# Kernel optimization log

Hardware: AMD Instinct MI355X
Metric: run time of the kernel (lower is better)

The kernel has to match this reference:

```python
import jax, jax.numpy as jnp
import numpy as np

N, E = 32, 512          # graphs per batch, padded nodes per graph
IN_DIM = 128            # in_dim
OUT_DIM = 64            # out_dim (d)
N_TYPE = 3              # config.num_edge_type
Q_DIM = 128             # config.input_dim (q_update=False)


def setup_inputs() -> dict:
    key = jax.random.key(0)
    ks = jax.random.split(key, 8)
    s = 0.05  # weight init scale (stands in for xavier_uniform)
    return {
        "input_state": jax.random.normal(ks[0], (N, E, IN_DIM), jnp.float32),
        "adj": jax.random.randint(ks[1], (N, E, E), 0, N_TYPE + 1, jnp.int32),
        "query_vec": jax.random.normal(ks[2], (N, Q_DIM), jnp.float32),
        "node_mask": jax.random.uniform(ks[3], (N, E, 1), jnp.float32),
        "W_type": jax.random.normal(ks[4], (N_TYPE, IN_DIM, OUT_DIM), jnp.float32) * s,
        "a_type": jax.random.normal(ks[5], (N_TYPE, 2 * OUT_DIM, 1), jnp.float32) * s,
        "qattn_W1": jax.random.normal(ks[6], (N_TYPE, Q_DIM, 2 * OUT_DIM), jnp.float32) * s,
        "qattn_W2": jax.random.normal(ks[7], (N_TYPE, 2 * OUT_DIM, 2 * OUT_DIM), jnp.float32) * s,
    }


def reference(input_state, adj, query_vec, node_mask, W_type, a_type, qattn_W1, qattn_W2):
    # Per-type node projections: (T, N, E, d). Dropout omitted (eval mode, p=0).
    h_all = jnp.einsum("nei,tio->tneo", input_state, W_type)

    # Query gate per type: sigmoid(relu(q @ W1) @ W2) -> (T, N, 2d)
    qg = jax.nn.relu(jnp.einsum("nq,tqc->tnc", query_vec, qattn_W1))
    qg = jax.nn.sigmoid(jnp.einsum("tnc,tcd->tnd", qg, qattn_W2))

    d = h_all.shape[-1]
    a_src = a_type[:, :d, 0]   # (T, d) applied to the repeated (source) half
    a_dst = a_type[:, d:, 0]   # (T, d) applied to the tiled (target) half

    # score[t,n,i,j] = lrelu( (h[t,n,i]*qg1[t,n]) . a_src[t] + (h[t,n,j]*qg2[t,n]) . a_dst[t] )
    # This is exactly cat([h_i, h_j]) * q_gate @ a without materializing (N,E,E,2d).
    s_src = jnp.einsum("tned,tnd,td->tne", h_all, qg[..., :d], a_src)
    s_dst = jnp.einsum("tned,tnd,td->tne", h_all, qg[..., d:], a_dst)
    score = jax.nn.leaky_relu(s_src[:, :, :, None] + s_dst[:, :, None, :], 0.2)  # (T,N,E,E)

    # Accumulate scores where adj matches each edge type (1-indexed).
    type_ids = jnp.arange(1, N_TYPE + 1, dtype=adj.dtype)[:, None, None, None]
    scores = jnp.sum(jnp.where(adj[None] == type_ids, score, 0.0), axis=0)  # (N,E,E)

    # Mask non-edges and softmax over dim=2 (target nodes).
    scores = jnp.where(adj > 0, scores, jnp.float32(-1e30))
    coefs = jax.nn.softmax(scores, axis=2)

    # h from the last edge-type loop iteration, node-masked.
    h = h_all[-1] * node_mask  # (N,E,d)

    # out[n,j,:] = sum_i coefs[n,i,j] * h[n,i,:]  (sum over dim=1 in the torch code)
    return jnp.einsum("nij,nid->njd", coefs, h)
```

## Files before the change

kernel.cpp:

```cpp
#include <hip/hip_runtime.h>
#include <hip/hip_bf16.h>

#define N_G 32
#define E_N 512
#define IN_D 128
#define OUT_D 64
#define NT 3
#define Q_D 128

#define WS_WSRC 0
#define WS_WDST 12288
#define WS_SSRC 24576
#define WS_SDST 73728
#define WS_RINV 139264
#define WS_H    155648
#define WS_W2T  679936
#define WS_ADJ2 684032

typedef const float* fp;
typedef __attribute__((ext_vector_type(8))) short short8x;
typedef __attribute__((ext_vector_type(4))) float float4x;

static __device__ inline ushort f2bf(float x) {
  __hip_bfloat16 b = __float2bfloat16(x);
  return *(ushort*)&b;
}
static __device__ inline float bf2f(ushort u) {
  return __uint_as_float((uint)u << 16);
}

__global__ __launch_bounds__(512) void k1_qgate(fp qv_g, fp Wt, fp at,
                                                fp W1, fp W2,
                                                float* __restrict__ ws) {
  const int tb = blockIdx.x >> 5;
  const int n  = blockIdx.x & 31;
  __shared__ float qv[128];
  __shared__ float ps[16][132];
  __shared__ float g1s[128], g2s[128];
  __shared__ float gsv[64], gdv[64];
  const int t  = threadIdx.x;
  const int h  = t >> 5;
  const int cg = (t & 31) << 2;

  if (t < 128) qv[t] = qv_g[n * Q_D + t];
  __syncthreads();

  {
    float a0 = 0.f, a1 = 0.f, a2 = 0.f, a3 = 0.f;
    const float* Wp = W1 + tb * 16384 + (h * 8) * 128 + cg;
    #pragma unroll
    for (int q = 0; q < 8; q++) {
      float4 wv = *(const float4*)(Wp + q * 128);
      float qq = qv[h * 8 + q];
      a0 += qq * wv.x; a1 += qq * wv.y; a2 += qq * wv.z; a3 += qq * wv.w;
    }
    ps[h][cg + 0] = a0; ps[h][cg + 1] = a1;
    ps[h][cg + 2] = a2; ps[h][cg + 3] = a3;
  }
  __syncthreads();
  if (t < 128) {
    float s = 0.f;
    #pragma unroll
    for (int k = 0; k < 16; k++) s += ps[k][t];
    g1s[t] = s > 0.f ? s : 0.f;
  }
  __syncthreads();

  {
    float a0 = 0.f, a1 = 0.f, a2 = 0.f, a3 = 0.f;
    const float* Wp = W2 + tb * 16384 + (h * 8) * 128 + cg;
    #pragma unroll
    for (int q = 0; q < 8; q++) {
      float4 wv = *(const float4*)(Wp + q * 128);
      float qq = g1s[h * 8 + q];
      a0 += qq * wv.x; a1 += qq * wv.y; a2 += qq * wv.z; a3 += qq * wv.w;
    }
    ps[h][cg + 0] = a0; ps[h][cg + 1] = a1;
    ps[h][cg + 2] = a2; ps[h][cg + 3] = a3;
  }
  __syncthreads();
  if (t < 128) {
    float s = 0.f;
    #pragma unroll
    for (int k = 0; k < 16; k++) s += ps[k][t];
    g2s[t] = 1.f / (1.f + __expf(-s));
  }
  __syncthreads();
  if (t < 64) {
    gsv[t] = g2s[t] * at[tb * 128 + t];
    gdv[t] = g2s[64 + t] * at[tb * 128 + 64 + t];
  }
  __syncthreads();

  if (t < 256) {
    const int i = t & 127, hf = t >> 7;
    float as = 0.f, ad = 0.f;
    const float* Wp = Wt + tb * 8192 + i * 64 + hf * 32;
    #pragma unroll
    for (int dj = 0; dj < 8; dj++) {
      float4 wv = *(const float4*)(Wp + dj * 4);
      const float* gp = gsv + hf * 32 + dj * 4;
      const float* gq = gdv + hf * 32 + dj * 4;
      as += wv.x * gp[0] + wv.y * gp[1] + wv.z * gp[2] + wv.w * gp[3];
      ad += wv.x * gq[0] + wv.y * gq[1] + wv.z * gq[2] + wv.w * gq[3];
    }
    ps[hf][i]     = as;
    ps[2 + hf][i] = ad;
  }
  __syncthreads();
  if (t < 128) {
    ws[WS_WSRC + tb * 4096 + n * 128 + t] = ps[0][t] + ps[1][t];
    ws[WS_WDST + tb * 4096 + n * 128 + t] = ps[2][t] + ps[3][t];
  }

  if (tb == 2 && t < 128) {
    int f = n * 256 + t * 2;
    int d = f >> 7, i0 = f & 127;
    uint lo = f2bf(Wt[2 * 8192 + i0 * 64 + d]);
    uint hi = f2bf(Wt[2 * 8192 + (i0 + 1) * 64 + d]);
    ((uint*)(ws + WS_W2T))[f >> 1] = lo | (hi << 16);
  }
}

__global__ __launch_bounds__(256) void k2_h_s(fp X, fp mask,
                                              float* __restrict__ ws) {
  const int n  = blockIdx.x >> 4;
  const int e0 = (blockIdx.x & 15) << 5;
  __shared__ ushort A[32 * 136];
  __shared__ ushort BT[64 * 136];
  __shared__ ushort eT[64 * 40];
  __shared__ float wv[6 * 128];
  const int t = threadIdx.x;
  ushort* hb = (ushort*)(ws + WS_H);
  const ushort* w2t = (const ushort*)(ws + WS_W2T);

  #pragma unroll
  for (int k = 0; k < 4; k++) {
    int f = t + 256 * k;
    int e = f >> 5, iq = f & 31;
    float4 v = *(const float4*)&X[(n * E_N + e0 + e) * IN_D + iq * 4];
    uint2 pk;
    pk.x = (uint)f2bf(v.x) | ((uint)f2bf(v.y) << 16);
    pk.y = (uint)f2bf(v.z) | ((uint)f2bf(v.w) << 16);
    *(uint2*)&A[e * 136 + iq * 4] = pk;
  }
  #pragma unroll
  for (int k = 0; k < 4; k++) {
    int f = t + 256 * k;
    int d = f >> 4, iq8 = f & 15;
    *(uint4*)&BT[d * 136 + iq8 * 8] = *(const uint4*)&w2t[d * 128 + iq8 * 8];
  }
  #pragma unroll
  for (int k = 0; k < 3; k++) {
    int idx = t + 256 * k;
    int row = idx >> 7, i = idx & 127;
    wv[idx] = (row < 3) ? ws[WS_WSRC + row * 4096 + n * 128 + i]
                        : ws[WS_WDST + (row - 3) * 4096 + n * 128 + i];
  }
  __syncthreads();

  const int w = t >> 6, lane = t & 63;
  const int m15 = lane & 15, quad = lane >> 4;
  const int msub = w & 1, dhalf = w >> 1;

  float4x acc2[2];
  acc2[0] = (float4x)(0.f); acc2[1] = (float4x)(0.f);
  #pragma unroll
  for (int ks = 0; ks < 4; ks++) {
    short8x af = *(const short8x*)&A[(msub * 16 + m15) * 136 + ks * 32 + quad * 8];
    #pragma unroll
    for (int dd = 0; dd < 2; dd++) {
      short8x bfv = *(const short8x*)&BT[((dhalf * 2 + dd) * 16 + m15) * 136 + ks * 32 + quad * 8];
      acc2[dd] = __builtin_amdgcn_mfma_f32_16x16x32_bf16(af, bfv, acc2[dd], 0, 0, 0);
    }
  }

  if (t < 192) {
    const int e = t / 6, q = t % 6;
    float acc = 0.f;
    #pragma unroll
    for (int i8 = 0; i8 < 16; i8++) {
      uint4 pk = *(const uint4*)&A[e * 136 + i8 * 8];
      const float* wp = &wv[q * 128 + i8 * 8];
      acc += bf2f((ushort)(pk.x & 0xffff)) * wp[0];
      acc += bf2f((ushort)(pk.x >> 16))    * wp[1];
      acc += bf2f((ushort)(pk.y & 0xffff)) * wp[2];
      acc += bf2f((ushort)(pk.y >> 16))    * wp[3];
      acc += bf2f((ushort)(pk.z & 0xffff)) * wp[4];
      acc += bf2f((ushort)(pk.z >> 16))    * wp[5];
      acc += bf2f((ushort)(pk.w & 0xffff)) * wp[6];
      acc += bf2f((ushort)(pk.w >> 16))    * wp[7];
    }
    if (q < 3) ws[WS_SSRC + q * 16384 + n * 512 + e0 + e] = acc;
    else       ws[WS_SDST + (q - 3) * 16384 + n * 512 + e0 + e] = acc;
  }

  float mv[4];
  #pragma unroll
  for (int rg = 0; rg < 4; rg++)
    mv[rg] = mask[n * E_N + e0 + msub * 16 + quad * 4 + rg];
  #pragma unroll
  for (int dd = 0; dd < 2; dd++) {
    int dRow = (dhalf * 2 + dd) * 16 + m15;
    #pragma unroll
    for (int rg = 0; rg < 4; rg++) {
      int e = msub * 16 + quad * 4 + rg;
      eT[dRow * 40 + e] = f2bf(acc2[dd][rg] * mv[rg]);
    }
  }
  __syncthreads();

  {
    int d = t >> 2, e8 = t & 3;
    *(uint4*)&hb[(n * 64 + d) * 512 + e0 + e8 * 8] =
        *(const uint4*)&eT[d * 40 + e8 * 8];
  }
}

__global__ __launch_bounds__(256) void k3_rowstats(const int* __restrict__ adj,
                                                   float* __restrict__ ws) {
  const int n  = blockIdx.x >> 7;
  const int ib = blockIdx.x & 127;
  __shared__ float sd[3 * 512];
  const int t = threadIdx.x;
  ushort* adj2 = (ushort*)(ws + WS_ADJ2);

  #pragma unroll
  for (int k = 0; k < 6; k++) {
    int idx = t + 256 * k;
    sd[idx] = ws[WS_SDST + (idx >> 9) * 16384 + n * 512 + (idx & 511)];
  }
  __syncthreads();

  const int wave = t >> 6, lane = t & 63;
  const int i = ib * 4 + wave;
  const float s0 = ws[WS_SSRC + 0 * 16384 + n * 512 + i];
  const float s1 = ws[WS_SSRC + 1 * 16384 + n * 512 + i];
  const float s2 = ws[WS_SSRC + 2 * 16384 + n * 512 + i];
  const int* arow = &adj[(n * E_N + i) * E_N];

  float sum = 0.f;
  uint pack = 0;
  #pragma unroll
  for (int b = 0; b < 8; b++) {
    int j = b * 64 + lane;
    int a = arow[j];
    pack |= (uint)(a & 3) << (2 * b);
    if (a > 0) {
      float s = (a == 1) ? s0 : (a == 2 ? s1 : s2);
      float v = s + sd[(a - 1) * 512 + j];
      v = v > 0.f ? v : 0.2f * v;
      sum += __expf(v);
    }
  }
  #pragma unroll
  for (int off = 32; off >= 1; off >>= 1) sum += __shfl_xor(sum, off, 64);
  if (lane == 0) ws[WS_RINV + n * 512 + i] = 1.f / sum;
  adj2[(n * E_N + i) * 64 + lane] = (ushort)pack;
}

__global__ __launch_bounds__(256) void k4_out(float* __restrict__ ws,
                                              float* __restrict__ out) {
  const int n  = blockIdx.x >> 4;
  const int j0 = (blockIdx.x & 15) << 5;
  __shared__ ushort cT[32 * 136];
  __shared__ ushort hT[64 * 136];
  __shared__ ushort aS[128 * 64];
  __shared__ float sdT[3 * 32];
  __shared__ float ssT[3 * 128];
  __shared__ float riT[128];
  const int t = threadIdx.x;
  const ushort* hb = (const ushort*)(ws + WS_H);
  const ushort* adj2 = (const ushort*)(ws + WS_ADJ2);

  if (t < 96) sdT[t] = ws[WS_SDST + (t >> 5) * 16384 + n * 512 + j0 + (t & 31)];

  const int w = t >> 6, lane = t & 63;
  const int m15 = lane & 15, quad = lane >> 4;
  const int msub = w & 1, dhalf = w >> 1;
  const int c   = t & 31;
  const int rpb = t >> 5;
  const int u     = (j0 & 63) + c;
  const int shift = 2 * (j0 >> 6);

  float4x acc[2];
  acc[0] = (float4x)(0.f); acc[1] = (float4x)(0.f);

  for (int it = 0; it < 4; it++) {
    const int i0 = it << 7;

    #pragma unroll
    for (int k = 0; k < 4; k++) {
      int f = t + 256 * k;
      int d = f >> 4, i16 = f & 15;
      *(uint4*)&hT[d * 136 + i16 * 8] =
          *(const uint4*)&hb[(n * 64 + d) * 512 + i0 + i16 * 8];
    }
    #pragma unroll
    for (int k = 0; k < 4; k++) {
      int f = t + 256 * k;
      int r = f >> 3, c8 = f & 7;
      *(uint4*)&aS[r * 64 + c8 * 8] =
          *(const uint4*)&adj2[(size_t)(n * E_N + i0 + r) * 64 + c8 * 8];
    }
    #pragma unroll
    for (int k = 0; k < 2; k++) {
      int idx = t + 256 * k;
      if (idx < 128) riT[idx] = ws[WS_RINV + n * 512 + i0 + idx];
      else {
        int j2 = idx - 128;
        ssT[j2] = ws[WS_SSRC + (j2 >> 7) * 16384 + n * 512 + i0 + (j2 & 127)];
      }
    }
    __syncthreads();

    #pragma unroll
    for (int k = 0; k < 8; k++) {
      int r0 = 2 * (rpb + 8 * k);
      uint pack = 0;
      int a = (aS[r0 * 64 + u] >> shift) & 3;
      if (a > 0) {
        float v = ssT[(a - 1) * 128 + r0] + sdT[(a - 1) * 32 + c];
        v = v > 0.f ? v : 0.2f * v;
        pack = f2bf(__expf(v) * riT[r0]);
      }
      a = (aS[(r0 + 1) * 64 + u] >> shift) & 3;
      if (a > 0) {
        float v = ssT[(a - 1) * 128 + r0 + 1] + sdT[(a - 1) * 32 + c];
        v = v > 0.f ? v : 0.2f * v;
        pack |= (uint)f2bf(__expf(v) * riT[r0 + 1]) << 16;
      }
      *(uint*)&cT[c * 136 + r0] = pack;
    }
    __syncthreads();

    #pragma unroll
    for (int ks = 0; ks < 4; ks++) {
      short8x af = *(const short8x*)&cT[(msub * 16 + m15) * 136 + ks * 32 + quad * 8];
      #pragma unroll
      for (int dd = 0; dd < 2; dd++) {
        short8x bfv = *(const short8x*)&hT[((dhalf * 2 + dd) * 16 + m15) * 136 + ks * 32 + quad * 8];
        acc[dd] = __builtin_amdgcn_mfma_f32_16x16x32_bf16(af, bfv, acc[dd], 0, 0, 0);
      }
    }
    __syncthreads();
  }

  #pragma unroll
  for (int dd = 0; dd < 2; dd++)
    #pragma unroll
    for (int rg = 0; rg < 4; rg++) {
      int j = j0 + msub * 16 + quad * 4 + rg;
      out[(n * E_N + j) * 64 + (dhalf * 2 + dd) * 16 + m15] = acc[dd][rg];
    }
}

extern "C" void kernel_launch(void* const* d_in, const int* in_sizes, int n_in,
                              void* d_out, int out_size, void* d_ws, size_t ws_size,
                              hipStream_t stream) {
  fp input_state  = (fp)d_in[0];
  const int* adj  = (const int*)d_in[1];
  fp query_vec    = (fp)d_in[2];
  fp node_mask    = (fp)d_in[3];
  fp W_type       = (fp)d_in[4];
  fp a_type       = (fp)d_in[5];
  fp qattn_W1     = (fp)d_in[6];
  fp qattn_W2     = (fp)d_in[7];
  float* out = (float*)d_out;
  float* ws  = (float*)d_ws;

  k1_qgate<<<96, 512, 0, stream>>>(query_vec, W_type, a_type, qattn_W1, qattn_W2, ws);
  k2_h_s<<<512, 256, 0, stream>>>(input_state, node_mask, ws);
  k3_rowstats<<<32 * 128, 256, 0, stream>>>(adj, ws);
  k4_out<<<32 * 16, 256, 0, stream>>>(ws, out);
}
```

Baseline: 123.6 us.

## Fuse four stage kernels into one cooperative kernel with grid-wide barriers

New measurement: 448.2 us. 263% more time.

```diff
diff --git a/kernel.cpp b/kernel.cpp
--- a/kernel.cpp
+++ b/kernel.cpp
@@ -1,5 +1,8 @@
 #include <hip/hip_runtime.h>
 #include <hip/hip_bf16.h>
+#include <hip/hip_cooperative_groups.h>
+
+namespace cgx = cooperative_groups;
 
 #define N_G 32
 #define E_N 512
@@ -29,348 +32,362 @@
   return __uint_as_float((uint)u << 16);
 }
 
-__global__ __launch_bounds__(512) void k1_qgate(fp qv_g, fp Wt, fp at,
-                                                fp W1, fp W2,
-                                                float* __restrict__ ws) {
-  const int tb = blockIdx.x >> 5;
-  const int n  = blockIdx.x & 31;
-  __shared__ float qv[128];
-  __shared__ float ps[16][132];
-  __shared__ float g1s[128], g2s[128];
-  __shared__ float gsv[64], gdv[64];
-  const int t  = threadIdx.x;
-  const int h  = t >> 5;
-  const int cg = (t & 31) << 2;
-
-  if (t < 128) qv[t] = qv_g[n * Q_D + t];
-  __syncthreads();
+__global__ __launch_bounds__(256, 2) void fused_gat(
+    fp X, const int* __restrict__ adj, fp qv_g, fp mask,
+    fp Wt, fp at, fp W1, fp W2,
+    float* __restrict__ out, float* __restrict__ ws) {
+  cgx::grid_group grid = cgx::this_grid();
+  __shared__ alignas(16) char smem[45056];
+  const int b = blockIdx.x;
+  const int t = threadIdx.x;
+
+  if (b < 96) {
+    const int tb = b >> 5;
+    const int n  = b & 31;
+    float* qv  = (float*)smem;
+    float* ps  = (float*)(smem + 512);
+    float* g1s = (float*)(smem + 4736);
+    float* g2s = (float*)(smem + 5248);
+    float* gsv = (float*)(smem + 5760);
+    float* gdv = (float*)(smem + 6016);
+    const int h   = t >> 5;
+    const int cg_ = (t & 31) << 2;
+
+    if (t < 128) qv[t] = qv_g[n * Q_D + t];
+    __syncthreads();
+
+    {
+      float a0 = 0.f, a1 = 0.f, a2 = 0.f, a3 = 0.f;
+      const float* Wp = W1 + tb * 16384 + (h * 16) * 128 + cg_;
+      #pragma unroll
+      for (int q = 0; q < 16; q++) {
+        float4 wv4 = *(const float4*)(Wp + q * 128);
+        float qq = qv[h * 16 + q];
+        a0 += qq * wv4.x; a1 += qq * wv4.y; a2 += qq * wv4.z; a3 += qq * wv4.w;
+      }
+      ps[h * 132 + cg_ + 0] = a0; ps[h * 132 + cg_ + 1] = a1;
+      ps[h * 132 + cg_ + 2] = a2; ps[h * 132 + cg_ + 3] = a3;
+    }
+    __syncthreads();
+    if (t < 128) {
+      float s = 0.f;
+      #pragma unroll
+      for (int k = 0; k < 8; k++) s += ps[k * 132 + t];
+      g1s[t] = s > 0.f ? s : 0.f;
+    }
+    __syncthreads();
+
+    {
+      float a0 = 0.f, a1 = 0.f, a2 = 0.f, a3 = 0.f;
+      const float* Wp = W2 + tb * 16384 + (h * 16) * 128 + cg_;
+      #pragma unroll
+      for (int q = 0; q < 16; q++) {
+        float4 wv4 = *(const float4*)(Wp + q * 128);
+        float qq = g1s[h * 16 + q];
+        a0 += qq * wv4.x; a1 += qq * wv4.y; a2 += qq * wv4.z; a3 += qq * wv4.w;
+      }
+      ps[h * 132 + cg_ + 0] = a0; ps[h * 132 + cg_ + 1] = a1;
+      ps[h * 132 + cg_ + 2] = a2; ps[h * 132 + cg_ + 3] = a3;
+    }
+    __syncthreads();
+    if (t < 128) {
+      float s = 0.f;
+      #pragma unroll
+      for (int k = 0; k < 8; k++) s += ps[k * 132 + t];
+      g2s[t] = 1.f / (1.f + __expf(-s));
+    }
+    __syncthreads();
+    if (t < 64) {
+      gsv[t] = g2s[t] * at[tb * 128 + t];
+      gdv[t] = g2s[64 + t] * at[tb * 128 + 64 + t];
+    }
+    __syncthreads();
+
+    {
+      const int i = t & 127, hf = t >> 7;
+      float as = 0.f, ad = 0.f;
+      const float* Wp = Wt + tb * 8192 + i * 64 + hf * 32;
+      #pragma unroll
+      for (int dj = 0; dj < 8; dj++) {
+        float4 wv4 = *(const float4*)(Wp + dj * 4);
+        const float* gp = gsv + hf * 32 + dj * 4;
+        const float* gq = gdv + hf * 32 + dj * 4;
+        as += wv4.x * gp[0] + wv4.y * gp[1] + wv4.z * gp[2] + wv4.w * gp[3];
+        ad += wv4.x * gq[0] + wv4.y * gq[1] + wv4.z * gq[2] + wv4.w * gq[3];
+      }
+      ps[hf * 132 + i]       = as;
+      ps[(2 + hf) * 132 + i] = ad;
+    }
+    __syncthreads();
+    if (t < 128) {
+      ws[WS_WSRC + tb * 4096 + n * 128 + t] = ps[0 * 132 + t] + ps[1 * 132 + t];
+      ws[WS_WDST + tb * 4096 + n * 128 + t] = ps[2 * 132 + t] + ps[3 * 132 + t];
+    }
+    if (tb == 2 && t < 128) {
+      int f = n * 256 + t * 2;
+      int d = f >> 7, i0 = f & 127;
+      uint lo = f2bf(Wt[2 * 8192 + i0 * 64 + d]);
+      uint hi = f2bf(Wt[2 * 8192 + (i0 + 1) * 64 + d]);
+      ((uint*)(ws + WS_W2T))[f >> 1] = lo | (hi << 16);
+    }
+  }
+
+  __threadfence();
+  grid.sync();
 
   {
-    float a0 = 0.f, a1 = 0.f, a2 = 0.f, a3 = 0.f;
-    const float* Wp = W1 + tb * 16384 + (h * 8) * 128 + cg;
-    #pragma unroll
-    for (int q = 0; q < 8; q++) {
-      float4 wv = *(const float4*)(Wp + q * 128);
-      float qq = qv[h * 8 + q];
-      a0 += qq * wv.x; a1 += qq * wv.y; a2 += qq * wv.z; a3 += qq * wv.w;
-    }
-    ps[h][cg + 0] = a0; ps[h][cg + 1] = a1;
-    ps[h][cg + 2] = a2; ps[h][cg + 3] = a3;
-  }
-  __syncthreads();
-  if (t < 128) {
-    float s = 0.f;
-    #pragma unroll
-    for (int k = 0; k < 16; k++) s += ps[k][t];
-    g1s[t] = s > 0.f ? s : 0.f;
-  }
-  __syncthreads();
-
-  {
-    float a0 = 0.f, a1 = 0.f, a2 = 0.f, a3 = 0.f;
-    const float* Wp = W2 + tb * 16384 + (h * 8) * 128 + cg;
-    #pragma unroll
-    for (int q = 0; q < 8; q++) {
-      float4 wv = *(const float4*)(Wp + q * 128);
-      float qq = g1s[h * 8 + q];
-      a0 += qq * wv.x; a1 += qq * wv.y; a2 += qq * wv.z; a3 += qq * wv.w;
-    }
-    ps[h][cg + 0] = a0; ps[h][cg + 1] = a1;
-    ps[h][cg + 2] = a2; ps[h][cg + 3] = a3;
-  }
-  __syncthreads();
-  if (t < 128) {
-    float s = 0.f;
-    #pragma unroll
-    for (int k = 0; k < 16; k++) s += ps[k][t];
-    g2s[t] = 1.f / (1.f + __expf(-s));
-  }
-  __syncthreads();
-  if (t < 64) {
-    gsv[t] = g2s[t] * at[tb * 128 + t];
-    gdv[t] = g2s[64 + t] * at[tb * 128 + 64 + t];
-  }
-  __syncthreads();
-
-  if (t < 256) {
-    const int i = t & 127, hf = t >> 7;
-    float as = 0.f, ad = 0.f;
-    const float* Wp = Wt + tb * 8192 + i * 64 + hf * 32;
-    #pragma unroll
-    for (int dj = 0; dj < 8; dj++) {
-      float4 wv = *(const float4*)(Wp + dj * 4);
-      const float* gp = gsv + hf * 32 + dj * 4;
-      const float* gq = gdv + hf * 32 + dj * 4;
-      as += wv.x * gp[0] + wv.y * gp[1] + wv.z * gp[2] + wv.w * gp[3];
-      ad += wv.x * gq[0] + wv.y * gq[1] + wv.z * gq[2] + wv.w * gq[3];
-    }
-    ps[hf][i]     = as;
-    ps[2 + hf][i] = ad;
-  }
-  __syncthreads();
-  if (t < 128) {
-    ws[WS_WSRC + tb * 4096 + n * 128 + t] = ps[0][t] + ps[1][t];
-    ws[WS_WDST + tb * 4096 + n * 128 + t] = ps[2][t] + ps[3][t];
-  }
-
-  if (tb == 2 && t < 128) {
-    int f = n * 256 + t * 2;
-    int d = f >> 7, i0 = f & 127;
-    uint lo = f2bf(Wt[2 * 8192 + i0 * 64 + d]);
-    uint hi = f2bf(Wt[2 * 8192 + (i0 + 1) * 64 + d]);
-    ((uint*)(ws + WS_W2T))[f >> 1] = lo | (hi << 16);
-  }
-}
-
-__global__ __launch_bounds__(256) void k2_h_s(fp X, fp mask,
-                                              float* __restrict__ ws) {
-  const int n  = blockIdx.x >> 4;
-  const int e0 = (blockIdx.x & 15) << 5;
-  __shared__ ushort A[32 * 136];
-  __shared__ ushort BT[64 * 136];
-  __shared__ ushort eT[64 * 40];
-  __shared__ float wv[6 * 128];
-  const int t = threadIdx.x;
-  ushort* hb = (ushort*)(ws + WS_H);
-  const ushort* w2t = (const ushort*)(ws + WS_W2T);
-
-  #pragma unroll
-  for (int k = 0; k < 4; k++) {
-    int f = t + 256 * k;
-    int e = f >> 5, iq = f & 31;
-    float4 v = *(const float4*)&X[(n * E_N + e0 + e) * IN_D + iq * 4];
-    uint2 pk;
-    pk.x = (uint)f2bf(v.x) | ((uint)f2bf(v.y) << 16);
-    pk.y = (uint)f2bf(v.z) | ((uint)f2bf(v.w) << 16);
-    *(uint2*)&A[e * 136 + iq * 4] = pk;
-  }
-  #pragma unroll
-  for (int k = 0; k < 4; k++) {
-    int f = t + 256 * k;
-    int d = f >> 4, iq8 = f & 15;
-    *(uint4*)&BT[d * 136 + iq8 * 8] = *(const uint4*)&w2t[d * 128 + iq8 * 8];
-  }
-  #pragma unroll
-  for (int k = 0; k < 3; k++) {
-    int idx = t + 256 * k;
-    int row = idx >> 7, i = idx & 127;
-    wv[idx] = (row < 3) ? ws[WS_WSRC + row * 4096 + n * 128 + i]
-                        : ws[WS_WDST + (row - 3) * 4096 + n * 128 + i];
-  }
-  __syncthreads();
-
-  const int w = t >> 6, lane = t & 63;
-  const int m15 = lane & 15, quad = lane >> 4;
-  const int msub = w & 1, dhalf = w >> 1;
-
-  float4x acc2[2];
-  acc2[0] = (float4x)(0.f); acc2[1] = (float4x)(0.f);
-  #pragma unroll
-  for (int ks = 0; ks < 4; ks++) {
-    short8x af = *(const short8x*)&A[(msub * 16 + m15) * 136 + ks * 32 + quad * 8];
-    #pragma unroll
-    for (int dd = 0; dd < 2; dd++) {
-      short8x bfv = *(const short8x*)&BT[((dhalf * 2 + dd) * 16 + m15) * 136 + ks * 32 + quad * 8];
-      acc2[dd] = __builtin_amdgcn_mfma_f32_16x16x32_bf16(af, bfv, acc2[dd], 0, 0, 0);
-    }
-  }
-
-  if (t < 192) {
-    const int e = t / 6, q = t % 6;
-    float acc = 0.f;
-    #pragma unroll
-    for (int i8 = 0; i8 < 16; i8++) {
-      uint4 pk = *(const uint4*)&A[e * 136 + i8 * 8];
-      const float* wp = &wv[q * 128 + i8 * 8];
-      acc += bf2f((ushort)(pk.x & 0xffff)) * wp[0];
-      acc += bf2f((ushort)(pk.x >> 16))    * wp[1];
-      acc += bf2f((ushort)(pk.y & 0xffff)) * wp[2];
-      acc += bf2f((ushort)(pk.y >> 16))    * wp[3];
-      acc += bf2f((ushort)(pk.z & 0xffff)) * wp[4];
-      acc += bf2f((ushort)(pk.z >> 16))    * wp[5];
-      acc += bf2f((ushort)(pk.w & 0xffff)) * wp[6];
-      acc += bf2f((ushort)(pk.w >> 16))    * wp[7];
-    }
-    if (q < 3) ws[WS_SSRC + q * 16384 + n * 512 + e0 + e] = acc;
-    else       ws[WS_SDST + (q - 3) * 16384 + n * 512 + e0 + e] = acc;
-  }
-
-  float mv[4];
-  #pragma unroll
-  for (int rg = 0; rg < 4; rg++)
-    mv[rg] = mask[n * E_N + e0 + msub * 16 + quad * 4 + rg];
-  #pragma unroll
-  for (int dd = 0; dd < 2; dd++) {
-    int dRow = (dhalf * 2 + dd) * 16 + m15;
-    #pragma unroll
-    for (int rg = 0; rg < 4; rg++) {
-      int e = msub * 16 + quad * 4 + rg;
-      eT[dRow * 40 + e] = f2bf(acc2[dd][rg] * mv[rg]);
-    }
-  }
-  __syncthreads();
-
-  {
-    int d = t >> 2, e8 = t & 3;
-    *(uint4*)&hb[(n * 64 + d) * 512 + e0 + e8 * 8] =
-        *(const uint4*)&eT[d * 40 + e8 * 8];
-  }
-}
-
-__global__ __launch_bounds__(256) void k3_rowstats(const int* __restrict__ adj,
-                                                   float* __restrict__ ws) {
-  const int n  = blockIdx.x >> 7;
-  const int ib = blockIdx.x & 127;
-  __shared__ float sd[3 * 512];
-  const int t = threadIdx.x;
-  ushort* adj2 = (ushort*)(ws + WS_ADJ2);
-
-  #pragma unroll
-  for (int k = 0; k < 6; k++) {
-    int idx = t + 256 * k;
-    sd[idx] = ws[WS_SDST + (idx >> 9) * 16384 + n * 512 + (idx & 511)];
-  }
-  __syncthreads();
-
-  const int wave = t >> 6, lane = t & 63;
-  const int i = ib * 4 + wave;
-  const float s0 = ws[WS_SSRC + 0 * 16384 + n * 512 + i];
-  const float s1 = ws[WS_SSRC + 1 * 16384 + n * 512 + i];
-  const float s2 = ws[WS_SSRC + 2 * 16384 + n * 512 + i];
-  const int* arow = &adj[(n * E_N + i) * E_N];
-
-  float sum = 0.f;
-  uint pack = 0;
-  #pragma unroll
-  for (int b = 0; b < 8; b++) {
-    int j = b * 64 + lane;
-    int a = arow[j];
-    pack |= (uint)(a & 3) << (2 * b);
-    if (a > 0) {
-      float s = (a == 1) ? s0 : (a == 2 ? s1 : s2);
-      float v = s + sd[(a - 1) * 512 + j];
-      v = v > 0.f ? v : 0.2f * v;
-      sum += __expf(v);
-    }
-  }
-  #pragma unroll
-  for (int off = 32; off >= 1; off >>= 1) sum += __shfl_xor(sum, off, 64);
-  if (lane == 0) ws[WS_RINV + n * 512 + i] = 1.f / sum;
-  adj2[(n * E_N + i) * 64 + lane] = (ushort)pack;
-}
-
-__global__ __launch_bounds__(256) void k4_out(float* __restrict__ ws,
-                                              float* __restrict__ out) {
-  const int n  = blockIdx.x >> 4;
-  const int j0 = (blockIdx.x & 15) << 5;
-  __shared__ ushort cT[32 * 136];
-  __shared__ ushort hT[64 * 136];
-  __shared__ ushort aS[128 * 64];
-  __shared__ float sdT[3 * 32];
-  __shared__ float ssT[3 * 128];
-  __shared__ float riT[128];
-  const int t = threadIdx.x;
-  const ushort* hb = (const ushort*)(ws + WS_H);
-  const ushort* adj2 = (const ushort*)(ws + WS_ADJ2);
-
-  if (t < 96) sdT[t] = ws[WS_SDST + (t >> 5) * 16384 + n * 512 + j0 + (t & 31)];
-
-  const int w = t >> 6, lane = t & 63;
-  const int m15 = lane & 15, quad = lane >> 4;
-  const int msub = w & 1, dhalf = w >> 1;
-  const int c   = t & 31;
-  const int rpb = t >> 5;
-  const int u     = (j0 & 63) + c;
-  const int shift = 2 * (j0 >> 6);
-
-  float4x acc[2];
-  acc[0] = (float4x)(0.f); acc[1] = (float4x)(0.f);
-
-  for (int it = 0; it < 4; it++) {
-    const int i0 = it << 7;
+    const int n  = b >> 4;
+    const int e0 = (b & 15) << 5;
+    ushort* A   = (ushort*)smem;
+    ushort* BT  = (ushort*)(smem + 8704);
+    ushort* eTl = (ushort*)(smem + 26112);
+    float*  wv  = (float*)(smem + 31232);
+    ushort* hb = (ushort*)(ws + WS_H);
+    const ushort* w2t = (const ushort*)(ws + WS_W2T);
 
     #pragma unroll
     for (int k = 0; k < 4; k++) {
       int f = t + 256 * k;
-      int d = f >> 4, i16 = f & 15;
-      *(uint4*)&hT[d * 136 + i16 * 8] =
-          *(const uint4*)&hb[(n * 64 + d) * 512 + i0 + i16 * 8];
+      int e = f >> 5, iq = f & 31;
+      float4 v = *(const float4*)&X[(n * E_N + e0 + e) * IN_D + iq * 4];
+      uint2 pk;
+      pk.x = (uint)f2bf(v.x) | ((uint)f2bf(v.y) << 16);
+      pk.y = (uint)f2bf(v.z) | ((uint)f2bf(v.w) << 16);
+      *(uint2*)&A[e * 136 + iq * 4] = pk;
     }
     #pragma unroll
     for (int k = 0; k < 4; k++) {
       int f = t + 256 * k;
-      int r = f >> 3, c8 = f & 7;
-      *(uint4*)&aS[r * 64 + c8 * 8] =
-          *(const uint4*)&adj2[(size_t)(n * E_N + i0 + r) * 64 + c8 * 8];
-    }
-    #pragma unroll
-    for (int k = 0; k < 2; k++) {
+      int d = f >> 4, iq8 = f & 15;
+      *(uint4*)&BT[d * 136 + iq8 * 8] = *(const uint4*)&w2t[d * 128 + iq8 * 8];
+    }
+    #pragma unroll
+    for (int k = 0; k < 3; k++) {
       int idx = t + 256 * k;
-      if (idx < 128) riT[idx] = ws[WS_RINV + n * 512 + i0 + idx];
-      else {
-        int j2 = idx - 128;
-        ssT[j2] = ws[WS_SSRC + (j2 >> 7) * 16384 + n * 512 + i0 + (j2 & 127)];
-      }
-    }
-    __syncthreads();
-
-    #pragma unroll
-    for (int k = 0; k < 8; k++) {
-      int r0 = 2 * (rpb + 8 * k);
+      int row = idx >> 7, i = idx & 127;
+      wv[idx] = (row < 3) ? ws[WS_WSRC + row * 4096 + n * 128 + i]
+                          : ws[WS_WDST + (row - 3) * 4096 + n * 128 + i];
+    }
+    __syncthreads();
+
+    const int w = t >> 6, lane = t & 63;
+    const int m15 = lane & 15, quad = lane >> 4;
+    const int msub = w & 1, dhalf = w >> 1;
+
+    float4x acc2[2];
+    acc2[0] = (float4x)(0.f); acc2[1] = (float4x)(0.f);
+    #pragma unroll
+    for (int ks = 0; ks < 4; ks++) {
+      short8x af = *(const short8x*)&A[(msub * 16 + m15) * 136 + ks * 32 + quad * 8];
+      #pragma unroll
+      for (int dd = 0; dd < 2; dd++) {
+        short8x bfv = *(const short8x*)&BT[((dhalf * 2 + dd) * 16 + m15) * 136 + ks * 32 + quad * 8];
+        acc2[dd] = __builtin_amdgcn_mfma_f32_16x16x32_bf16(af, bfv, acc2[dd], 0, 0, 0);
+      }
+    }
+
+    if (t < 192) {
+      const int e = t / 6, q = t % 6;
+      float acc = 0.f;
+      #pragma unroll
+      for (int i8 = 0; i8 < 16; i8++) {
+        uint4 pk = *(const uint4*)&A[e * 136 + i8 * 8];
+        const float* wp = &wv[q * 128 + i8 * 8];
+        acc += bf2f((ushort)(pk.x & 0xffff)) * wp[0];
+        acc += bf2f((ushort)(pk.x >> 16))    * wp[1];
+        acc += bf2f((ushort)(pk.y & 0xffff)) * wp[2];
+        acc += bf2f((ushort)(pk.y >> 16))    * wp[3];
+        acc += bf2f((ushort)(pk.z & 0xffff)) * wp[4];
+        acc += bf2f((ushort)(pk.z >> 16))    * wp[5];
+        acc += bf2f((ushort)(pk.w & 0xffff)) * wp[6];
+        acc += bf2f((ushort)(pk.w >> 16))    * wp[7];
+      }
+      if (q < 3) ws[WS_SSRC + q * 16384 + n * 512 + e0 + e] = acc;
+      else       ws[WS_SDST + (q - 3) * 16384 + n * 512 + e0 + e] = acc;
+    }
+
+    float mv[4];
+    #pragma unroll
+    for (int rg = 0; rg < 4; rg++)
+      mv[rg] = mask[n * E_N + e0 + msub * 16 + quad * 4 + rg];
+    #pragma unroll
+    for (int dd = 0; dd < 2; dd++) {
+      int dRow = (dhalf * 2 + dd) * 16 + m15;
+      #pragma unroll
+      for (int rg = 0; rg < 4; rg++) {
+        int e = msub * 16 + quad * 4 + rg;
+        eTl[dRow * 40 + e] = f2bf(acc2[dd][rg] * mv[rg]);
+      }
+    }
+    __syncthreads();
+
+    {
+      int d = t >> 2, e8 = t & 3;
+      *(uint4*)&hb[(n * 64 + d) * 512 + e0 + e8 * 8] =
+          *(const uint4*)&eTl[d * 40 + e8 * 8];
+    }
+  }
+
+  __threadfence();
+  grid.sync();
+
+  {
+    const int n  = b >> 4;
+    const int rb = (b & 15) << 5;
+    float* sd = (float*)smem;
+    ushort* adj2 = (ushort*)(ws + WS_ADJ2);
+
+    #pragma unroll
+    for (int k = 0; k < 6; k++) {
+      int idx = t + 256 * k;
+      sd[idx] = ws[WS_SDST + (idx >> 9) * 16384 + n * 512 + (idx & 511)];
+    }
+    __syncthreads();
+
+    const int wave = t >> 6, lane = t & 63;
+    for (int rr = 0; rr < 8; rr++) {
+      const int i = rb + wave * 8 + rr;
+      const float s0 = ws[WS_SSRC + 0 * 16384 + n * 512 + i];
+      const float s1 = ws[WS_SSRC + 1 * 16384 + n * 512 + i];
+      const float s2 = ws[WS_SSRC + 2 * 16384 + n * 512 + i];
+      const int* arow = &adj[(n * E_N + i) * E_N];
+
+      float sum = 0.f;
       uint pack = 0;
-      int a = (aS[r0 * 64 + u] >> shift) & 3;
-      if (a > 0) {
-        float v = ssT[(a - 1) * 128 + r0] + sdT[(a - 1) * 32 + c];
-        v = v > 0.f ? v : 0.2f * v;
-        pack = f2bf(__expf(v) * riT[r0]);
-      }
-      a = (aS[(r0 + 1) * 64 + u] >> shift) & 3;
-      if (a > 0) {
-        float v = ssT[(a - 1) * 128 + r0 + 1] + sdT[(a - 1) * 32 + c];
-        v = v > 0.f ? v : 0.2f * v;
-        pack |= (uint)f2bf(__expf(v) * riT[r0 + 1]) << 16;
-      }
-      *(uint*)&cT[c * 136 + r0] = pack;
-    }
-    __syncthreads();
-
-    #pragma unroll
-    for (int ks = 0; ks < 4; ks++) {
-      short8x af = *(const short8x*)&cT[(msub * 16 + m15) * 136 + ks * 32 + quad * 8];
-      #pragma unroll
-      for (int dd = 0; dd < 2; dd++) {
-        short8x bfv = *(const short8x*)&hT[((dhalf * 2 + dd) * 16 + m15) * 136 + ks * 32 + quad * 8];
-        acc[dd] = __builtin_amdgcn_mfma_f32_16x16x32_bf16(af, bfv, acc[dd], 0, 0, 0);
-      }
-    }
-    __syncthreads();
+      #pragma unroll
+      for (int bb = 0; bb < 8; bb++) {
+        int j = bb * 64 + lane;
+        int a = arow[j];
+        pack |= (uint)(a & 3) << (2 * bb);
+        if (a > 0) {
+          float s = (a == 1) ? s0 : (a == 2 ? s1 : s2);
+          float v = s + sd[(a - 1) * 512 + j];
+          v = v > 0.f ? v : 0.2f * v;
+          sum += __expf(v);
+        }
+      }
+      #pragma unroll
+      for (int off = 32; off >= 1; off >>= 1) sum += __shfl_xor(sum, off, 64);
+      if (lane == 0) ws[WS_RINV + n * 512 + i] = 1.f / sum;
+      adj2[(n * E_N + i) * 64 + lane] = (ushort)pack;
+    }
   }
 
-  #pragma unroll
-  for (int dd = 0; dd < 2; dd++)
-    #pragma unroll
-    for (int rg = 0; rg < 4; rg++) {
-      int j = j0 + msub * 16 + quad * 4 + rg;
-      out[(n * E_N + j) * 64 + (dhalf * 2 + dd) * 16 + m15] = acc[dd][rg];
-    }
+  __threadfence();
+  grid.sync();
+
+  {
+    const int n  = b >> 4;
+    const int j0 = (b & 15) << 5;
+    ushort* cT = (ushort*)smem;
+    ushort* hT = (ushort*)(smem + 8704);
+    ushort* aS = (ushort*)(smem + 26112);
+    float* sdT = (float*)(smem + 42496);
+    float* ssT = (float*)(smem + 42880);
+    float* riT = (float*)(smem + 44416);
+    const ushort* hb = (const ushort*)(ws + WS_H);
+    const ushort* adj2 = (const ushort*)(ws + WS_ADJ2);
+
+    if (t < 96) sdT[t] = ws[WS_SDST + (t >> 5) * 16384 + n * 512 + j0 + (t & 31)];
+
+    const int w = t >> 6, lane = t & 63;
+    const int m15 = lane & 15, quad = lane >> 4;
+    const int msub = w & 1, dhalf = w >> 1;
+    const int c   = t & 31;
+    const int rpb = t >> 5;
+    const int u     = (j0 & 63) + c;
+    const int shift = 2 * (j0 >> 6);
+
+    float4x acc[2];
+    acc[0] = (float4x)(0.f); acc[1] = (float4x)(0.f);
+
+    for (int it = 0; it < 4; it++) {
+      const int i0 = it << 7;
+
+      #pragma unroll
+      for (int k = 0; k < 4; k++) {
+        int f = t + 256 * k;
+        int d = f >> 4, i16 = f & 15;
+        *(uint4*)&hT[d * 136 + i16 * 8] =
+            *(const uint4*)&hb[(n * 64 + d) * 512 + i0 + i16 * 8];
+      }
+      #pragma unroll
+      for (int k = 0; k < 4; k++) {
+        int f = t + 256 * k;
+        int r = f >> 3, c8 = f & 7;
+        *(uint4*)&aS[r * 64 + c8 * 8] =
+            *(const uint4*)&adj2[(size_t)(n * E_N + i0 + r) * 64 + c8 * 8];
+      }
+      #pragma unroll
+      for (int k = 0; k < 2; k++) {
+        int idx = t + 256 * k;
+        if (idx < 128) riT[idx] = ws[WS_RINV + n * 512 + i0 + idx];
+        else {
+          int j2 = idx - 128;
+          ssT[j2] = ws[WS_SSRC + (j2 >> 7) * 16384 + n * 512 + i0 + (j2 & 127)];
+        }
+      }
+      __syncthreads();
+
+      #pragma unroll
+      for (int k = 0; k < 8; k++) {
+        int r0 = 2 * (rpb + 8 * k);
+        uint pack = 0;
+        int a = (aS[r0 * 64 + u] >> shift) & 3;
+        if (a > 0) {
+          float v = ssT[(a - 1) * 128 + r0] + sdT[(a - 1) * 32 + c];
+          v = v > 0.f ? v : 0.2f * v;
+          pack = f2bf(__expf(v) * riT[r0]);
+        }
+        a = (aS[(r0 + 1) * 64 + u] >> shift) & 3;
+        if (a > 0) {
+          float v = ssT[(a - 1) * 128 + r0 + 1] + sdT[(a - 1) * 32 + c];
+          v = v > 0.f ? v : 0.2f * v;
+          pack |= (uint)f2bf(__expf(v) * riT[r0 + 1]) << 16;
+        }
+        *(uint*)&cT[c * 136 + r0] = pack;
+      }
+      __syncthreads();
+
+      #pragma unroll
+      for (int ks = 0; ks < 4; ks++) {
+        short8x af = *(const short8x*)&cT[(msub * 16 + m15) * 136 + ks * 32 + quad * 8];
+        #pragma unroll
+        for (int dd = 0; dd < 2; dd++) {
+          short8x bfv = *(const short8x*)&hT[((dhalf * 2 + dd) * 16 + m15) * 136 + ks * 32 + quad * 8];
+          acc[dd] = __builtin_amdgcn_mfma_f32_16x16x32_bf16(af, bfv, acc[dd], 0, 0, 0);
+        }
+      }
+      __syncthreads();
+    }
+
+    #pragma unroll
+    for (int dd = 0; dd < 2; dd++)
+      #pragma unroll
+      for (int rg = 0; rg < 4; rg++) {
+        int j = j0 + msub * 16 + quad * 4 + rg;
+        out[(n * E_N + j) * 64 + (dhalf * 2 + dd) * 16 + m15] = acc[dd][rg];
+      }
+  }
 }
 
 extern "C" void kernel_launch(void* const* d_in, const int* in_sizes, int n_in,
                               void* d_out, int out_size, void* d_ws, size_t ws_size,
                               hipStream_t stream) {
-  fp input_state  = (fp)d_in[0];
-  const int* adj  = (const int*)d_in[1];
-  fp query_vec    = (fp)d_in[2];
-  fp node_mask    = (fp)d_in[3];
-  fp W_type       = (fp)d_in[4];
-  fp a_type       = (fp)d_in[5];
-  fp qattn_W1     = (fp)d_in[6];
-  fp qattn_W2     = (fp)d_in[7];
+  const float* input_state = (const float*)d_in[0];
+  const int*   adj         = (const int*)d_in[1];
+  const float* query_vec   = (const float*)d_in[2];
+  const float* node_mask   = (const float*)d_in[3];
+  const float* W_type      = (const float*)d_in[4];
+  const float* a_type      = (const float*)d_in[5];
+  const float* qattn_W1    = (const float*)d_in[6];
+  const float* qattn_W2    = (const float*)d_in[7];
   float* out = (float*)d_out;
   float* ws  = (float*)d_ws;
 
-  k1_qgate<<<96, 512, 0, stream>>>(query_vec, W_type, a_type, qattn_W1, qattn_W2, ws);
-  k2_h_s<<<512, 256, 0, stream>>>(input_state, node_mask, ws);
-  k3_rowstats<<<32 * 128, 256, 0, stream>>>(adj, ws);
-  k4_out<<<32 * 16, 256, 0, stream>>>(ws, out);
+  void* args[] = {(void*)&input_state, (void*)&adj, (void*)&query_vec,
+                  (void*)&node_mask, (void*)&W_type, (void*)&a_type,
+                  (void*)&qattn_W1, (void*)&qattn_W2, (void*)&out, (void*)&ws};
+  hipLaunchCooperativeKernel((const void*)fused_gat, dim3(512), dim3(256),
+                             args, 0, stream);
 }
```

## Move adjacency packing into qgate kernel and batch row stats per block

Applied to the files above, without the earlier changes.

Result: slower. 128.2 us (+3.7%).

```diff
diff --git a/kernel.cpp b/kernel.cpp
--- a/kernel.cpp
+++ b/kernel.cpp
@@ -29,60 +29,76 @@
   return __uint_as_float((uint)u << 16);
 }
 
-__global__ __launch_bounds__(512) void k1_qgate(fp qv_g, fp Wt, fp at,
-                                                fp W1, fp W2,
-                                                float* __restrict__ ws) {
-  const int tb = blockIdx.x >> 5;
-  const int n  = blockIdx.x & 31;
+__global__ __launch_bounds__(256) void k1_qgate_pack(
+    fp qv_g, fp Wt, fp at, fp W1, fp W2,
+    const int* __restrict__ adj, float* __restrict__ ws) {
+  const int b = blockIdx.x;
+  const int t = threadIdx.x;
+
+  if (b >= 96) {
+    const int w = t >> 6, lane = t & 63;
+    const int R = (b - 96) * 4 + w;
+    const int* arow = adj + (size_t)R * E_N;
+    uint pack = 0;
+    #pragma unroll
+    for (int bb = 0; bb < 8; bb++) {
+      int a = arow[bb * 64 + lane];
+      pack |= (uint)(a & 3) << (2 * bb);
+    }
+    ((ushort*)(ws + WS_ADJ2))[(size_t)R * 64 + lane] = (ushort)pack;
+    return;
+  }
+
+  const int tb = b >> 5;
+  const int n  = b & 31;
   __shared__ float qv[128];
-  __shared__ float ps[16][132];
+  __shared__ float ps[8][132];
   __shared__ float g1s[128], g2s[128];
   __shared__ float gsv[64], gdv[64];
-  const int t  = threadIdx.x;
-  const int h  = t >> 5;
-  const int cg = (t & 31) << 2;
+  const int h   = t >> 5;
+  const int cg_ = (t & 31) << 2;
 
   if (t < 128) qv[t] = qv_g[n * Q_D + t];
   __syncthreads();
 
   {
     float a0 = 0.f, a1 = 0.f, a2 = 0.f, a3 = 0.f;
-    const float* Wp = W1 + tb * 16384 + (h * 8) * 128 + cg;
-    #pragma unroll
-    for (int q = 0; q < 8; q++) {
-      float4 wv = *(const float4*)(Wp + q * 128);
-      float qq = qv[h * 8 + q];
-      a0 += qq * wv.x; a1 += qq * wv.y; a2 += qq * wv.z; a3 += qq * wv.w;
-    }
-    ps[h][cg + 0] = a0; ps[h][cg + 1] = a1;
-    ps[h][cg + 2] = a2; ps[h][cg + 3] = a3;
+    const float* Wp = W1 + tb * 16384 + (h * 16) * 128 + cg_;
+    #pragma unroll
+    for (int q = 0; q < 16; q++) {
+      float4 wv4 = *(const float4*)(Wp + q * 128);
+      float qq = qv[h * 16 + q];
+      a0 += qq * wv4.x; a1 += qq * wv4.y; a2 += qq * wv4.z; a3 += qq * wv4.w;
+    }
+    ps[h][cg_ + 0] = a0; ps[h][cg_ + 1] = a1;
+    ps[h][cg_ + 2] = a2; ps[h][cg_ + 3] = a3;
   }
   __syncthreads();
   if (t < 128) {
     float s = 0.f;
     #pragma unroll
-    for (int k = 0; k < 16; k++) s += ps[k][t];
+    for (int k = 0; k < 8; k++) s += ps[k][t];
     g1s[t] = s > 0.f ? s : 0.f;
   }
   __syncthreads();
 
   {
     float a0 = 0.f, a1 = 0.f, a2 = 0.f, a3 = 0.f;
-    const float* Wp = W2 + tb * 16384 + (h * 8) * 128 + cg;
-    #pragma unroll
-    for (int q = 0; q < 8; q++) {
-      float4 wv = *(const float4*)(Wp + q * 128);
-      float qq = g1s[h * 8 + q];
-      a0 += qq * wv.x; a1 += qq * wv.y; a2 += qq * wv.z; a3 += qq * wv.w;
-    }
-    ps[h][cg + 0] = a0; ps[h][cg + 1] = a1;
-    ps[h][cg + 2] = a2; ps[h][cg + 3] = a3;
+    const float* Wp = W2 + tb * 16384 + (h * 16) * 128 + cg_;
+    #pragma unroll
+    for (int q = 0; q < 16; q++) {
+      float4 wv4 = *(const float4*)(Wp + q * 128);
+      float qq = g1s[h * 16 + q];
+      a0 += qq * wv4.x; a1 += qq * wv4.y; a2 += qq * wv4.z; a3 += qq * wv4.w;
+    }
+    ps[h][cg_ + 0] = a0; ps[h][cg_ + 1] = a1;
+    ps[h][cg_ + 2] = a2; ps[h][cg_ + 3] = a3;
   }
   __syncthreads();
   if (t < 128) {
     float s = 0.f;
     #pragma unroll
-    for (int k = 0; k < 16; k++) s += ps[k][t];
+    for (int k = 0; k < 8; k++) s += ps[k][t];
     g2s[t] = 1.f / (1.f + __expf(-s));
   }
   __syncthreads();
@@ -92,17 +108,17 @@
   }
   __syncthreads();
 
-  if (t < 256) {
+  {
     const int i = t & 127, hf = t >> 7;
     float as = 0.f, ad = 0.f;
     const float* Wp = Wt + tb * 8192 + i * 64 + hf * 32;
     #pragma unroll
     for (int dj = 0; dj < 8; dj++) {
-      float4 wv = *(const float4*)(Wp + dj * 4);
+      float4 wv4 = *(const float4*)(Wp + dj * 4);
       const float* gp = gsv + hf * 32 + dj * 4;
       const float* gq = gdv + hf * 32 + dj * 4;
-      as += wv.x * gp[0] + wv.y * gp[1] + wv.z * gp[2] + wv.w * gp[3];
-      ad += wv.x * gq[0] + wv.y * gq[1] + wv.z * gq[2] + wv.w * gq[3];
+      as += wv4.x * gp[0] + wv4.y * gp[1] + wv4.z * gp[2] + wv4.w * gp[3];
+      ad += wv4.x * gq[0] + wv4.y * gq[1] + wv4.z * gq[2] + wv4.w * gq[3];
     }
     ps[hf][i]     = as;
     ps[2 + hf][i] = ad;
@@ -112,7 +128,6 @@
     ws[WS_WSRC + tb * 4096 + n * 128 + t] = ps[0][t] + ps[1][t];
     ws[WS_WDST + tb * 4096 + n * 128 + t] = ps[2][t] + ps[3][t];
   }
-
   if (tb == 2 && t < 128) {
     int f = n * 256 + t * 2;
     int d = f >> 7, i0 = f & 127;
@@ -124,8 +139,8 @@
 
 __global__ __launch_bounds__(256) void k2_h_s(fp X, fp mask,
                                               float* __restrict__ ws) {
-  const int n  = blockIdx.x >> 4;
-  const int e0 = (blockIdx.x & 15) << 5;
+  const int n  = blockIdx.x & 31;
+  const int e0 = (blockIdx.x >> 5) << 5;
   __shared__ ushort A[32 * 136];
   __shared__ ushort BT[64 * 136];
   __shared__ ushort eT[64 * 40];
@@ -217,13 +232,12 @@
   }
 }
 
-__global__ __launch_bounds__(256) void k3_rowstats(const int* __restrict__ adj,
-                                                   float* __restrict__ ws) {
-  const int n  = blockIdx.x >> 7;
-  const int ib = blockIdx.x & 127;
+__global__ __launch_bounds__(256) void k3_rows(float* __restrict__ ws) {
+  const int n  = blockIdx.x & 31;
+  const int rb = (blockIdx.x >> 5) << 5;
   __shared__ float sd[3 * 512];
   const int t = threadIdx.x;
-  ushort* adj2 = (ushort*)(ws + WS_ADJ2);
+  const ushort* adj2 = (const ushort*)(ws + WS_ADJ2);
 
   #pragma unroll
   for (int k = 0; k < 6; k++) {
@@ -233,36 +247,35 @@
   __syncthreads();
 
   const int wave = t >> 6, lane = t & 63;
-  const int i = ib * 4 + wave;
-  const float s0 = ws[WS_SSRC + 0 * 16384 + n * 512 + i];
-  const float s1 = ws[WS_SSRC + 1 * 16384 + n * 512 + i];
-  const float s2 = ws[WS_SSRC + 2 * 16384 + n * 512 + i];
-  const int* arow = &adj[(n * E_N + i) * E_N];
-
-  float sum = 0.f;
-  uint pack = 0;
-  #pragma unroll
-  for (int b = 0; b < 8; b++) {
-    int j = b * 64 + lane;
-    int a = arow[j];
-    pack |= (uint)(a & 3) << (2 * b);
-    if (a > 0) {
-      float s = (a == 1) ? s0 : (a == 2 ? s1 : s2);
-      float v = s + sd[(a - 1) * 512 + j];
-      v = v > 0.f ? v : 0.2f * v;
-      sum += __expf(v);
-    }
-  }
-  #pragma unroll
-  for (int off = 32; off >= 1; off >>= 1) sum += __shfl_xor(sum, off, 64);
-  if (lane == 0) ws[WS_RINV + n * 512 + i] = 1.f / sum;
-  adj2[(n * E_N + i) * 64 + lane] = (ushort)pack;
+  #pragma unroll
+  for (int rr = 0; rr < 8; rr++) {
+    const int i = rb + wave * 8 + rr;
+    const float s0 = ws[WS_SSRC + 0 * 16384 + n * 512 + i];
+    const float s1 = ws[WS_SSRC + 1 * 16384 + n * 512 + i];
+    const float s2 = ws[WS_SSRC + 2 * 16384 + n * 512 + i];
+    uint pk = adj2[(size_t)(n * E_N + i) * 64 + lane];
+
+    float sum = 0.f;
+    #pragma unroll
+    for (int bb = 0; bb < 8; bb++) {
+      int a = (pk >> (2 * bb)) & 3;
+      if (a > 0) {
+        float s = (a == 1) ? s0 : (a == 2 ? s1 : s2);
+        float v = s + sd[(a - 1) * 512 + bb * 64 + lane];
+        v = v > 0.f ? v : 0.2f * v;
+        sum += __expf(v);
+      }
+    }
+    #pragma unroll
+    for (int off = 32; off >= 1; off >>= 1) sum += __shfl_xor(sum, off, 64);
+    if (lane == 0) ws[WS_RINV + n * 512 + i] = 1.f / sum;
+  }
 }
 
 __global__ __launch_bounds__(256) void k4_out(float* __restrict__ ws,
                                               float* __restrict__ out) {
-  const int n  = blockIdx.x >> 4;
-  const int j0 = (blockIdx.x & 15) << 5;
+  const int n  = blockIdx.x & 31;
+  const int j0 = (blockIdx.x >> 5) << 5;
   __shared__ ushort cT[32 * 136];
   __shared__ ushort hT[64 * 136];
   __shared__ ushort aS[128 * 64];
@@ -369,8 +382,9 @@
   float* out = (float*)d_out;
   float* ws  = (float*)d_ws;
 
-  k1_qgate<<<96, 512, 0, stream>>>(query_vec, W_type, a_type, qattn_W1, qattn_W2, ws);
+  k1_qgate_pack<<<96 + 4096, 256, 0, stream>>>(query_vec, W_type, a_type,
+                                               qattn_W1, qattn_W2, adj, ws);
   k2_h_s<<<512, 256, 0, stream>>>(input_state, node_mask, ws);
-  k3_rowstats<<<32 * 128, 256, 0, stream>>>(adj, ws);
-  k4_out<<<32 * 16, 256, 0, stream>>>(ws, out);
-}
+  k3_rows<<<512, 256, 0, stream>>>(ws);
+  k4_out<<<512, 256, 0, stream>>>(ws, out);
+}
```

## Move adjacency packing into qgate kernel and read packed adj in rowstats

Applied to the files above, without the earlier changes.

Measured after the change: 127.2 us. +3.0%, slower.

```diff
diff --git a/kernel.cpp b/kernel.cpp
--- a/kernel.cpp
+++ b/kernel.cpp
@@ -29,16 +29,32 @@
   return __uint_as_float((uint)u << 16);
 }
 
-__global__ __launch_bounds__(512) void k1_qgate(fp qv_g, fp Wt, fp at,
-                                                fp W1, fp W2,
-                                                float* __restrict__ ws) {
-  const int tb = blockIdx.x >> 5;
-  const int n  = blockIdx.x & 31;
+__global__ __launch_bounds__(512) void k1_qgate_pack(
+    fp qv_g, fp Wt, fp at, fp W1, fp W2,
+    const int* __restrict__ adj, float* __restrict__ ws) {
+  const int b = blockIdx.x;
+  const int t = threadIdx.x;
+
+  if (b >= 96) {
+    const int w = t >> 6, lane = t & 63;
+    const int R = (b - 96) * 8 + w;
+    const int* arow = adj + (size_t)R * E_N;
+    uint pack = 0;
+    #pragma unroll
+    for (int bb = 0; bb < 8; bb++) {
+      int a = arow[bb * 64 + lane];
+      pack |= (uint)(a & 3) << (2 * bb);
+    }
+    ((ushort*)(ws + WS_ADJ2))[(size_t)R * 64 + lane] = (ushort)pack;
+    return;
+  }
+
+  const int tb = b >> 5;
+  const int n  = b & 31;
   __shared__ float qv[128];
   __shared__ float ps[16][132];
   __shared__ float g1s[128], g2s[128];
   __shared__ float gsv[64], gdv[64];
-  const int t  = threadIdx.x;
   const int h  = t >> 5;
   const int cg = (t & 31) << 2;
 
@@ -217,13 +233,12 @@
   }
 }
 
-__global__ __launch_bounds__(256) void k3_rowstats(const int* __restrict__ adj,
-                                                   float* __restrict__ ws) {
-  const int n  = blockIdx.x >> 7;
-  const int ib = blockIdx.x & 127;
+__global__ __launch_bounds__(256) void k3_rows(float* __restrict__ ws) {
+  const int n  = blockIdx.x >> 4;
+  const int rb = (blockIdx.x & 15) << 5;
   __shared__ float sd[3 * 512];
   const int t = threadIdx.x;
-  ushort* adj2 = (ushort*)(ws + WS_ADJ2);
+  const ushort* adj2 = (const ushort*)(ws + WS_ADJ2);
 
   #pragma unroll
   for (int k = 0; k < 6; k++) {
@@ -233,30 +248,29 @@
   __syncthreads();
 
   const int wave = t >> 6, lane = t & 63;
-  const int i = ib * 4 + wave;
-  const float s0 = ws[WS_SSRC + 0 * 16384 + n * 512 + i];
-  const float s1 = ws[WS_SSRC + 1 * 16384 + n * 512 + i];
-  const float s2 = ws[WS_SSRC + 2 * 16384 + n * 512 + i];
-  const int* arow = &adj[(n * E_N + i) * E_N];
-
-  float sum = 0.f;
-  uint pack = 0;
-  #pragma unroll
-  for (int b = 0; b < 8; b++) {
-    int j = b * 64 + lane;
-    int a = arow[j];
-    pack |= (uint)(a & 3) << (2 * b);
-    if (a > 0) {
-      float s = (a == 1) ? s0 : (a == 2 ? s1 : s2);
-      float v = s + sd[(a - 1) * 512 + j];
-      v = v > 0.f ? v : 0.2f * v;
-      sum += __expf(v);
-    }
-  }
-  #pragma unroll
-  for (int off = 32; off >= 1; off >>= 1) sum += __shfl_xor(sum, off, 64);
-  if (lane == 0) ws[WS_RINV + n * 512 + i] = 1.f / sum;
-  adj2[(n * E_N + i) * 64 + lane] = (ushort)pack;
+  #pragma unroll
+  for (int rr = 0; rr < 8; rr++) {
+    const int i = rb + wave * 8 + rr;
+    const float s0 = ws[WS_SSRC + 0 * 16384 + n * 512 + i];
+    const float s1 = ws[WS_SSRC + 1 * 16384 + n * 512 + i];
+    const float s2 = ws[WS_SSRC + 2 * 16384 + n * 512 + i];
+    uint pk = adj2[(size_t)(n * E_N + i) * 64 + lane];
+
+    float sum = 0.f;
+    #pragma unroll
+    for (int bb = 0; bb < 8; bb++) {
+      int a = (pk >> (2 * bb)) & 3;
+      if (a > 0) {
+        float s = (a == 1) ? s0 : (a == 2 ? s1 : s2);
+        float v = s + sd[(a - 1) * 512 + bb * 64 + lane];
+        v = v > 0.f ? v : 0.2f * v;
+        sum += __expf(v);
+      }
+    }
+    #pragma unroll
+    for (int off = 32; off >= 1; off >>= 1) sum += __shfl_xor(sum, off, 64);
+    if (lane == 0) ws[WS_RINV + n * 512 + i] = 1.f / sum;
+  }
 }
 
 __global__ __launch_bounds__(256) void k4_out(float* __restrict__ ws,
@@ -369,8 +383,9 @@
   float* out = (float*)d_out;
   float* ws  = (float*)d_ws;
 
-  k1_qgate<<<96, 512, 0, stream>>>(query_vec, W_type, a_type, qattn_W1, qattn_W2, ws);
+  k1_qgate_pack<<<96 + 2048, 512, 0, stream>>>(query_vec, W_type, a_type,
+                                               qattn_W1, qattn_W2, adj, ws);
   k2_h_s<<<512, 256, 0, stream>>>(input_state, node_mask, ws);
-  k3_rowstats<<<32 * 128, 256, 0, stream>>>(adj, ws);
+  k3_rows<<<512, 256, 0, stream>>>(ws);
   k4_out<<<32 * 16, 256, 0, stream>>>(ws, out);
 }
```
